# Optimization experiments

Measured on AMD Instinct MI355X. Metric: run time of the kernel, lower is better.

The kernel has to match this reference:

```python
import jax, jax.numpy as jnp
import numpy as np

NUM_ROUTING = 3

def _squash_elementwise(s):
    # Faithful to original: squared_norm summed over trailing dim of size 1,
    # i.e. elementwise: s^3 / ((1+s^2) * sqrt(s^2 + 1e-8))
    sq = s * s
    return sq * s / ((1.0 + sq) * jnp.sqrt(sq + 1e-8))

def setup_inputs() -> dict:
    key = jax.random.key(0)
    k1, k2 = jax.random.split(key)
    B, in_caps, in_dim, out_caps, out_dim = 64, 2048, 16, 32, 16
    x = jax.random.normal(k1, (B, in_caps, in_dim), dtype=jnp.float32)
    weight = jax.random.normal(k2, (in_caps, out_caps, out_dim, in_dim), dtype=jnp.float32)
    return {"x": x, "weight": weight}

def reference(x, weight):
    B, in_caps, _ = x.shape
    out_caps, out_dim = weight.shape[1], weight.shape[2]
    # u_hat[b,i,o,d] = sum_k W[i,o,d,k] * x[b,i,k]
    u_hat = jnp.einsum('iodk,bik->biod', weight, x)  # (B, in_caps, out_caps, out_dim)
    b_ij = jnp.zeros((B, in_caps, out_caps), dtype=x.dtype)
    v = None
    for it in range(NUM_ROUTING):
        c = jax.nn.softmax(b_ij, axis=2)                       # (B, in_caps, out_caps)
        s = jnp.einsum('bio,biod->bod', c, u_hat)              # (B, out_caps, out_dim)
        v = _squash_elementwise(s)
        if it < NUM_ROUTING - 1:
            a = jnp.einsum('biod,bod->bio', u_hat, v)          # agreement
            b_ij = b_ij + a
    return v[..., None]  # (B, out_caps, out_dim, 1) matching v_j.squeeze(1)
```

## Files before the change

### kernel.cpp

```cpp
#include <hip/hip_runtime.h>

#define IN_CAPS 2048
#define K_DIM   16
#define OD      512
#define NCH     64
#define ICH     32
#define ICH_U   8
#define NCH_U   (IN_CAPS / ICH_U)
#define NS0     32
#define ISL     (IN_CAPS / NS0)

__device__ __forceinline__ float dot4(const float4& a, const float4& b) {
    return fmaf(a.x, b.x, fmaf(a.y, b.y, fmaf(a.z, b.z, a.w * b.w)));
}

template<int BTILE>
__global__ __launch_bounds__(256, 4)
void k_uhat(const float* __restrict__ x,
            const float* __restrict__ W,
            float* __restrict__ u)
{
    const int t   = threadIdx.x;
    const int i0  = blockIdx.x * ICH_U;
    const int bl0 = blockIdx.y * BTILE;

    for (int ii = 0; ii < ICH_U; ++ii) {
        const int i = i0 + ii;
        const float4* wp = (const float4*)(W + ((size_t)i * OD + 2 * t) * K_DIM);
        const float4 w0a = wp[0], w0b = wp[1], w0c = wp[2], w0d = wp[3];
        const float4 w1a = wp[4], w1b = wp[5], w1c = wp[6], w1d = wp[7];
#pragma unroll
        for (int bb = 0; bb < BTILE; ++bb) {
            const float* xp = x + ((size_t)(bl0 + bb) * IN_CAPS + i) * K_DIM;
            const float4 xa = ((const float4*)xp)[0];
            const float4 xb = ((const float4*)xp)[1];
            const float4 xc = ((const float4*)xp)[2];
            const float4 xd = ((const float4*)xp)[3];
            float u0 = dot4(w0a, xa) + dot4(w0b, xb) + dot4(w0c, xc) + dot4(w0d, xd);
            float u1 = dot4(w1a, xa) + dot4(w1b, xb) + dot4(w1c, xc) + dot4(w1d, xd);
            ((float2*)(u + ((size_t)(bl0 + bb) * IN_CAPS + i) * OD))[t] =
                make_float2(u0, u1);
        }
    }
}

__global__ __launch_bounds__(256)
void k_s0(const float* __restrict__ u, float* __restrict__ part2)
{
    const int t  = threadIdx.x;
    const int sl = blockIdx.x;
    const int b  = blockIdx.y;
    const float* up = u + ((size_t)b * IN_CAPS + sl * ISL) * OD;
    float2 acc = make_float2(0.f, 0.f);
#pragma unroll 4
    for (int j = 0; j < ISL; ++j) {
        const float2 v = ((const float2*)(up + (size_t)j * OD))[t];
        acc.x += v.x; acc.y += v.y;
    }
    ((float2*)(part2 + ((size_t)b * NS0 + sl) * OD))[t] = acc;
}

template<bool FIRST>
__global__ __launch_bounds__(256)
void k_route(const float* __restrict__ u,
             const float* __restrict__ v,
             float* __restrict__ bij,
             float* __restrict__ part)
{
    const int t  = threadIdx.x;
    const int l  = t & 63;
    const int w  = t >> 6;
    const int ic = blockIdx.x;
    const int b  = blockIdx.y;
    const int o  = l >> 1;
    const int dh = l & 1;

    float vr[8];
    {
        const float* vp = v + (size_t)b * OD + o * 16 + dh * 8;
        const float4 va = *(const float4*)vp;
        const float4 vb = *(const float4*)(vp + 4);
        vr[0] = va.x; vr[1] = va.y; vr[2] = va.z; vr[3] = va.w;
        vr[4] = vb.x; vr[5] = vb.y; vr[6] = vb.z; vr[7] = vb.w;
    }
    float acc[8];
#pragma unroll
    for (int j = 0; j < 8; ++j) acc[j] = 0.f;

    const int ibase = ic * ICH + w * (ICH / 4);
    for (int ii = 0; ii < ICH / 4; ++ii) {
        const int i = ibase + ii;
        const float* up = u + ((size_t)b * IN_CAPS + i) * OD + l * 8;
        const float4 u0 = *(const float4*)up;
        const float4 u1 = *(const float4*)(up + 4);
        float uu[8] = {u0.x, u0.y, u0.z, u0.w, u1.x, u1.y, u1.z, u1.w};

        float ah = 0.f;
#pragma unroll
        for (int j = 0; j < 8; ++j) ah = fmaf(uu[j], vr[j], ah);
        float a = ah + __shfl_xor(ah, 1);

        float* bp = bij + ((size_t)b * IN_CAPS + i) * 32;
        if (FIRST) {
            if (dh == 0) bp[o] = a;
        } else {
            a += bp[o];
        }
        float m = a;
#pragma unroll
        for (int s = 1; s < 64; s <<= 1) m = fmaxf(m, __shfl_xor(m, s));
        const float e = __expf(a - m);
        float ssum = e;
#pragma unroll
        for (int s = 1; s < 64; s <<= 1) ssum += __shfl_xor(ssum, s);
        const float c = e * (2.f / ssum);
#pragma unroll
        for (int j = 0; j < 8; ++j) acc[j] = fmaf(c, uu[j], acc[j]);
    }

    __shared__ float red[4][OD];
#pragma unroll
    for (int j = 0; j < 8; ++j) red[w][l * 8 + j] = acc[j];
    __syncthreads();
    const float s0 = red[0][t] + red[1][t] + red[2][t] + red[3][t];
    const float s1 = red[0][t + 256] + red[1][t + 256] + red[2][t + 256] + red[3][t + 256];
    float* pp = part + ((size_t)b * NCH + ic) * OD;
    pp[t]       = s0;
    pp[t + 256] = s1;
}

template<int NC>
__global__ __launch_bounds__(256)
void k_reduce(const float* __restrict__ part, float* __restrict__ vout,
              float scale, int nb)
{
    const int idx = blockIdx.x * 256 + threadIdx.x;
    if (idx >= nb * OD) return;
    const int b  = idx >> 9;
    const int od = idx & (OD - 1);
    const float* p = part + (size_t)b * NC * OD + od;
    float s = 0.f;
#pragma unroll
    for (int ch = 0; ch < NC; ++ch) s += p[(size_t)ch * OD];
    s *= scale;
    const float sq = s * s;
    vout[idx] = sq * s / ((1.f + sq) * sqrtf(sq + 1e-8f));
}

extern "C" void kernel_launch(void* const* d_in, const int* in_sizes, int n_in,
                              void* d_out, int out_size, void* d_ws, size_t ws_size,
                              hipStream_t stream)
{
    const float* x = (const float*)d_in[0];
    const float* W = (const float*)d_in[1];
    float* out = (float*)d_out;

    const size_t U_B    = (size_t)IN_CAPS * OD * 4;
    const size_t BIJ_B  = (size_t)IN_CAPS * 32 * 4;
    const size_t PART_B = (size_t)NCH * OD * 4;
    const size_t V_B    = (size_t)OD * 4;
    const size_t PER_B  = U_B + BIJ_B + PART_B + 2 * V_B;

    int nb = 64;
    while (nb > 1 && (size_t)nb * PER_B > ws_size) nb >>= 1;
    if (nb > 32) nb = 32;

    char* wsc = (char*)d_ws;
    for (int b0 = 0; b0 < 64; b0 += nb) {
        float* u    = (float*)wsc;
        float* bij  = (float*)(wsc + (size_t)nb * U_B);
        float* part = (float*)(wsc + (size_t)nb * (U_B + BIJ_B));
        float* v0   = (float*)(wsc + (size_t)nb * (U_B + BIJ_B + PART_B));
        float* v1   = v0 + (size_t)nb * OD;

        const float* xb = x + (size_t)b0 * IN_CAPS * K_DIM;
        const int btile = (nb >= 8) ? 8 : ((nb >= 4) ? 4 : ((nb >= 2) ? 2 : 1));
        dim3 g1(NCH_U, nb / btile);
        switch (btile) {
            case 8: k_uhat<8><<<g1, 256, 0, stream>>>(xb, W, u); break;
            case 4: k_uhat<4><<<g1, 256, 0, stream>>>(xb, W, u); break;
            case 2: k_uhat<2><<<g1, 256, 0, stream>>>(xb, W, u); break;
            default: k_uhat<1><<<g1, 256, 0, stream>>>(xb, W, u); break;
        }
        const int rblocks = (nb * OD + 255) / 256;
        k_s0<<<dim3(NS0, nb), 256, 0, stream>>>(u, part);
        k_reduce<NS0><<<rblocks, 256, 0, stream>>>(part, v0, 1.f / 32.f, nb);
        k_route<true ><<<dim3(NCH, nb), 256, 0, stream>>>(u, v0, bij, part);
        k_reduce<NCH><<<rblocks, 256, 0, stream>>>(part, v1, 1.f, nb);
        k_route<false><<<dim3(NCH, nb), 256, 0, stream>>>(u, v1, bij, part);
        k_reduce<NCH><<<rblocks, 256, 0, stream>>>(part, out + (size_t)b0 * OD, 1.f, nb);
    }
}
```

Baseline: 261.3 us.

## Fuse first-iteration capsule sum into u_hat kernel via atomics, prefetch weights

The separate k_s0 pass, which re-read all of u_hat to form the uniform-coupling sum, is removed. k_uhat now accumulates per-thread partial sums while it computes u_hat and adds them into 32 slice buckets with atomicAdd, after a memset that zeroes the buffer. It also double-buffers the weight loads for the next input capsule. This saves one full read of the large u_hat buffer, at the cost of atomic traffic, nondeterministic summation order and higher register pressure from the extra accumulators and the second weight buffer.

```diff
diff --git a/kernel.cpp b/kernel.cpp
--- a/kernel.cpp
+++ b/kernel.cpp
@@ -8,7 +8,6 @@
 #define ICH_U   8
 #define NCH_U   (IN_CAPS / ICH_U)
 #define NS0     32
-#define ISL     (IN_CAPS / NS0)
 
 __device__ __forceinline__ float dot4(const float4& a, const float4& b) {
     return fmaf(a.x, b.x, fmaf(a.y, b.y, fmaf(a.z, b.z, a.w * b.w)));
@@ -18,17 +17,32 @@
 __global__ __launch_bounds__(256, 4)
 void k_uhat(const float* __restrict__ x,
             const float* __restrict__ W,
-            float* __restrict__ u)
+            float* __restrict__ u,
+            float* __restrict__ part)
 {
     const int t   = threadIdx.x;
-    const int i0  = blockIdx.x * ICH_U;
+    const int ib  = blockIdx.x;
+    const int i0  = ib * ICH_U;
     const int bl0 = blockIdx.y * BTILE;
+
+    float acc[2 * BTILE];
+#pragma unroll
+    for (int j = 0; j < 2 * BTILE; ++j) acc[j] = 0.f;
+
+    float4 wc[8], wn[8];
+    {
+        const float4* wp = (const float4*)(W + ((size_t)i0 * OD + 2 * t) * K_DIM);
+#pragma unroll
+        for (int q = 0; q < 8; ++q) wc[q] = wp[q];
+    }
 
     for (int ii = 0; ii < ICH_U; ++ii) {
         const int i = i0 + ii;
-        const float4* wp = (const float4*)(W + ((size_t)i * OD + 2 * t) * K_DIM);
-        const float4 w0a = wp[0], w0b = wp[1], w0c = wp[2], w0d = wp[3];
-        const float4 w1a = wp[4], w1b = wp[5], w1c = wp[6], w1d = wp[7];
+        if (ii + 1 < ICH_U) {
+            const float4* wp = (const float4*)(W + ((size_t)(i + 1) * OD + 2 * t) * K_DIM);
+#pragma unroll
+            for (int q = 0; q < 8; ++q) wn[q] = wp[q];
+        }
 #pragma unroll
         for (int bb = 0; bb < BTILE; ++bb) {
             const float* xp = x + ((size_t)(bl0 + bb) * IN_CAPS + i) * K_DIM;
@@ -36,28 +50,26 @@
             const float4 xb = ((const float4*)xp)[1];
             const float4 xc = ((const float4*)xp)[2];
             const float4 xd = ((const float4*)xp)[3];
-            float u0 = dot4(w0a, xa) + dot4(w0b, xb) + dot4(w0c, xc) + dot4(w0d, xd);
-            float u1 = dot4(w1a, xa) + dot4(w1b, xb) + dot4(w1c, xc) + dot4(w1d, xd);
+            float u0 = dot4(wc[0], xa) + dot4(wc[1], xb) + dot4(wc[2], xc) + dot4(wc[3], xd);
+            float u1 = dot4(wc[4], xa) + dot4(wc[5], xb) + dot4(wc[6], xc) + dot4(wc[7], xd);
+            acc[2 * bb]     += u0;
+            acc[2 * bb + 1] += u1;
             ((float2*)(u + ((size_t)(bl0 + bb) * IN_CAPS + i) * OD))[t] =
                 make_float2(u0, u1);
         }
-    }
-}
-
-__global__ __launch_bounds__(256)
-void k_s0(const float* __restrict__ u, float* __restrict__ part2)
-{
-    const int t  = threadIdx.x;
-    const int sl = blockIdx.x;
-    const int b  = blockIdx.y;
-    const float* up = u + ((size_t)b * IN_CAPS + sl * ISL) * OD;
-    float2 acc = make_float2(0.f, 0.f);
-#pragma unroll 4
-    for (int j = 0; j < ISL; ++j) {
-        const float2 v = ((const float2*)(up + (size_t)j * OD))[t];
-        acc.x += v.x; acc.y += v.y;
-    }
-    ((float2*)(part2 + ((size_t)b * NS0 + sl) * OD))[t] = acc;
+        if (ii + 1 < ICH_U) {
+#pragma unroll
+            for (int q = 0; q < 8; ++q) wc[q] = wn[q];
+        }
+    }
+
+    const int sl = ib & (NS0 - 1);
+#pragma unroll
+    for (int bb = 0; bb < BTILE; ++bb) {
+        float* pp = part + ((size_t)(bl0 + bb) * NS0 + sl) * OD + 2 * t;
+        atomicAdd(pp,     acc[2 * bb]);
+        atomicAdd(pp + 1, acc[2 * bb + 1]);
+    }
 }
 
 template<bool FIRST>
@@ -174,16 +186,18 @@
         float* v1   = v0 + (size_t)nb * OD;
 
         const float* xb = x + (size_t)b0 * IN_CAPS * K_DIM;
+
+        hipMemsetAsync(part, 0, (size_t)nb * NS0 * OD * 4, stream);
+
         const int btile = (nb >= 8) ? 8 : ((nb >= 4) ? 4 : ((nb >= 2) ? 2 : 1));
         dim3 g1(NCH_U, nb / btile);
         switch (btile) {
-            case 8: k_uhat<8><<<g1, 256, 0, stream>>>(xb, W, u); break;
-            case 4: k_uhat<4><<<g1, 256, 0, stream>>>(xb, W, u); break;
-            case 2: k_uhat<2><<<g1, 256, 0, stream>>>(xb, W, u); break;
-            default: k_uhat<1><<<g1, 256, 0, stream>>>(xb, W, u); break;
+            case 8: k_uhat<8><<<g1, 256, 0, stream>>>(xb, W, u, part); break;
+            case 4: k_uhat<4><<<g1, 256, 0, stream>>>(xb, W, u, part); break;
+            case 2: k_uhat<2><<<g1, 256, 0, stream>>>(xb, W, u, part); break;
+            default: k_uhat<1><<<g1, 256, 0, stream>>>(xb, W, u, part); break;
         }
         const int rblocks = (nb * OD + 255) / 256;
-        k_s0<<<dim3(NS0, nb), 256, 0, stream>>>(u, part);
         k_reduce<NS0><<<rblocks, 256, 0, stream>>>(part, v0, 1.f / 32.f, nb);
         k_route<true ><<<dim3(NCH, nb), 256, 0, stream>>>(u, v0, bij, part);
         k_reduce<NCH><<<rblocks, 256, 0, stream>>>(part, v1, 1.f, nb);
```

Result: slower. 287.6 us (+10.1%).
